# Kernel optimization log

Measured on AMD Instinct MI355X. Metric: run time of the kernel, lower is better.

## Reference

```python
import jax, jax.numpy as jnp
import numpy as np

B, L, D_MODEL, D_STATE, D_HIDDEN = 4, 4096, 1024, 256, 4096
RMIN, RMAX, MAX_PHASE = 0.8, 0.95, 2.0 * np.pi


def setup_inputs() -> dict:
    key = jax.random.key(0)
    ks = jax.random.split(key, 10)
    # LRU ring init (Orvieto et al.): |lambda| in [rmin, rmax], phase in [0, max_phase)
    u1 = jax.random.uniform(ks[0], (D_STATE,))
    u2 = jax.random.uniform(ks[1], (D_STATE,))
    nu_log = jnp.log(-0.5 * jnp.log(u1 * (RMAX**2 - RMIN**2) + RMIN**2))
    theta_log = jnp.log(MAX_PHASE * u2)
    B_re = jax.random.normal(ks[2], (D_STATE, D_MODEL)) / np.sqrt(2.0 * D_MODEL)
    B_im = jax.random.normal(ks[3], (D_STATE, D_MODEL)) / np.sqrt(2.0 * D_MODEL)
    C_re = jax.random.normal(ks[4], (D_MODEL, D_STATE)) / np.sqrt(D_STATE)
    C_im = jax.random.normal(ks[5], (D_MODEL, D_STATE)) / np.sqrt(D_STATE)
    D_mat = jax.random.normal(ks[6], (D_MODEL, D_MODEL)) / np.sqrt(D_MODEL)
    W1 = jax.random.normal(ks[7], (D_MODEL, D_HIDDEN)) * np.sqrt(2.0 / D_MODEL)
    W2 = jax.random.normal(ks[8], (D_HIDDEN, D_MODEL)) * np.sqrt(2.0 / D_HIDDEN)
    res_logit = jnp.asarray(-1.0, dtype=jnp.float32)
    x3d = jax.random.normal(ks[9], (B, L, D_MODEL), dtype=jnp.float32)
    return {"x3d": x3d, "nu_log": nu_log, "theta_log": theta_log,
            "B_re": B_re, "B_im": B_im, "C_re": C_re, "C_im": C_im,
            "D_mat": D_mat, "W1": W1, "W2": W2, "res_logit": res_logit}


def _lru_scan(lam, Bu):
    # diagonal linear recurrence x_t = lam * x_{t-1} + Bu_t via associative scan
    lam_b = jnp.broadcast_to(lam, Bu.shape)  # [B, L, N]

    def comb(a, b):
        return (a[0] * b[0], b[0] * a[1] + b[1])

    _, states = jax.lax.associative_scan(comb, (lam_b, Bu), axis=1)
    return states  # [B, L, N] complex


def reference(x3d, nu_log, theta_log, B_re, B_im, C_re, C_im, D_mat, W1, W2, res_logit):
    lam = jnp.exp(-jnp.exp(nu_log) + 1j * jnp.exp(theta_log))          # [N]
    gamma = jnp.sqrt(1.0 - jnp.abs(lam) ** 2)                           # [N]
    Bn = (gamma[:, None] * (B_re + 1j * B_im))                          # [N, D]
    Bu = jnp.einsum('bld,nd->bln', x3d.astype(jnp.complex64), Bn)       # [B, L, N]
    states = _lru_scan(lam.astype(jnp.complex64), Bu)                   # [B, L, N]
    y = jnp.einsum('bln,mn->blm', states, C_re + 1j * C_im).real \
        + jnp.einsum('bld,md->blm', x3d, D_mat)                         # [B, L, D]
    # MLP feedforward (nl_layers=2, bias=False), dropout is identity at p=0
    z = jax.nn.gelu(y @ W1) @ W2                                        # [B, L, D]
    out = x3d + jax.nn.sigmoid(res_logit) * z
    st = states[:, -1]  # final recurrent state
    return out, st
```

## Files before the change

kernel.cpp:

```cpp
#include <hip/hip_runtime.h>
#include <stdint.h>

typedef __bf16 bf16;
typedef bf16 bf16x8 __attribute__((ext_vector_type(8)));
typedef float f32x4 __attribute__((ext_vector_type(4)));

#define B_  4
#define L_  4096
#define DM  1024
#define DS  256
#define DH  4096
#define BL  16384
#define CL  64
#define NC  64

__device__ __forceinline__ float bfbits(uint32_t lo16) {
  union { uint32_t u; float f; } v; v.u = lo16 << 16; return v.f;
}

__device__ __forceinline__ void async16(const bf16* g, bf16* l) {
  __builtin_amdgcn_global_load_lds(
      (const __attribute__((address_space(1))) uint32_t*)g,
      (__attribute__((address_space(3))) uint32_t*)l, 16, 0, 0);
}

#define MEMFENCE()  asm volatile("" ::: "memory")
#define LGKM0()     asm volatile("s_waitcnt lgkmcnt(0)" ::: "memory")
#define SCHEDB()    __builtin_amdgcn_sched_barrier(0)

__global__ void phaseA(const float* __restrict__ nu_log,
                       const float* __restrict__ th_log,
                       float* __restrict__ scal) {
  int n = threadIdx.x;
  float nu = __expf(nu_log[n]);
  float th = __expf(th_log[n]);
  float mod = __expf(-nu);
  float lr = mod * cosf(th);
  float li = mod * sinf(th);
  float g = sqrtf(fmaxf(1.0f - mod * mod, 0.0f));
  float pr = 1.f, pi = 0.f;
  for (int i = 0; i < CL; i++) {
    float nr = pr * lr - pi * li;
    float ni = pr * li + pi * lr;
    pr = nr; pi = ni;
  }
  scal[n] = lr; scal[256 + n] = li;
  scal[512 + n] = pr; scal[768 + n] = pi;
  scal[1024 + n] = g;
}

__global__ void prep_bu(const float* __restrict__ B_re, const float* __restrict__ B_im,
                        const float* __restrict__ scal, bf16* __restrict__ WB) {
  size_t i = (size_t)blockIdx.x * 256 + threadIdx.x;
  int row = (int)(i >> 10), col = (int)(i & 1023);
  int n = row >> 1;
  const float* src = (row & 1) ? B_im : B_re;
  WB[i] = (bf16)(scal[1024 + n] * src[n * 1024 + col]);
}

__global__ void prep_y(const float* __restrict__ C_re, const float* __restrict__ C_im,
                       const float* __restrict__ D_mat, bf16* __restrict__ WB) {
  size_t i = (size_t)blockIdx.x * 256 + threadIdx.x;
  int m = (int)(i / 1536), c = (int)(i % 1536);
  float v;
  if (c < 256)       v = C_re[m * 256 + c];
  else if (c < 512)  v = -C_im[m * 256 + (c - 256)];
  else               v = D_mat[m * 1024 + (c - 512)];
  WB[i] = (bf16)v;
}

__global__ void transpose_to_bf16(const float* __restrict__ in, bf16* __restrict__ out,
                                  int R, int C) {
  __shared__ float tile[32][33];
  int c0 = blockIdx.x * 32, r0 = blockIdx.y * 32;
  int tx = threadIdx.x, ty = threadIdx.y;
  for (int i = 0; i < 32; i += 8)
    tile[ty + i][tx] = in[(size_t)(r0 + ty + i) * C + c0 + tx];
  __syncthreads();
  for (int i = 0; i < 32; i += 8)
    out[(size_t)(c0 + ty + i) * R + r0 + tx] = (bf16)tile[tx][ty + i];
}

__global__ void conv_x(const float4* __restrict__ x, bf16* __restrict__ XS) {
  size_t i = (size_t)blockIdx.x * 256 + threadIdx.x;
  size_t t = i >> 8;
  int d4 = (int)(i & 255);
  float4 v = x[i];
  bf16* o = XS + t * 1536 + 512 + (size_t)d4 * 4;
  o[0] = (bf16)v.x; o[1] = (bf16)v.y; o[2] = (bf16)v.z; o[3] = (bf16)v.w;
}

template <int EPI>
__device__ __forceinline__ void epi_store(void* C, int ldc, size_t row, size_t col,
                                          float v, float sig, const float* xres) {
  size_t off = row * (size_t)ldc + col;
  if (EPI == 0) {
    ((bf16*)C)[off] = (bf16)v;
  } else if (EPI == 1) {
    float z = 0.7978845608f * (v + 0.044715f * v * v * v);
    float gv = v / (1.f + __expf(-2.f * z));
    ((bf16*)C)[off] = (bf16)gv;
  } else {
    ((float*)C)[off] = xres[off] + sig * v;
  }
}

template <int EPI>
__global__ __launch_bounds__(512, 2) void gemm256(
    const bf16* __restrict__ A, int lda,
    const bf16* __restrict__ Bt, int ldb,
    void* __restrict__ C, int ldc, int NK, int mt, int nt,
    const float* __restrict__ xres, const float* __restrict__ reslog) {
  __shared__ __align__(16) bf16 sA[2 * 16384];
  __shared__ __align__(16) bf16 sB[2 * 16384];

  const int tid  = threadIdx.x;
  const int lane = tid & 63;
  const int wave = tid >> 6;
  const int q = lane >> 4, l16 = lane & 15;
  const int wr = wave >> 2, wc = wave & 3;

  int nb = mt * nt;
  int per = nb >> 3;
  int t0 = (blockIdx.x & 7) * per + (blockIdx.x >> 3);
  int gsz = nt << 3;
  int g = t0 / gsz, r = t0 % gsz;
  size_t m0 = (size_t)(g * 8 + (r & 7)) * 256;
  size_t n0 = (size_t)(r >> 3) * 256;

  const int srow = tid >> 3;
  const int scol = (((tid & 7) ^ ((tid >> 3) & 7)) << 3);
  const bf16* gA = A  + (m0 + srow) * (size_t)lda + scol;
  const bf16* gB = Bt + (n0 + srow) * (size_t)ldb + scol;
  bf16* lA = sA + tid * 8;
  bf16* lB = sB + tid * 8;

  auto stageA = [&](int kt) {
    const bf16* s = gA + kt * 64;
    bf16* l = lA + (kt & 1) * 16384;
    async16(s, l);
    async16(s + (size_t)64  * lda, l + 4096);
    async16(s + (size_t)128 * lda, l + 8192);
    async16(s + (size_t)192 * lda, l + 12288);
  };
  auto stageB = [&](int kt) {
    const bf16* s = gB + kt * 64;
    bf16* l = lB + (kt & 1) * 16384;
    async16(s, l);
    async16(s + (size_t)64  * ldb, l + 4096);
    async16(s + (size_t)128 * ldb, l + 8192);
    async16(s + (size_t)192 * ldb, l + 12288);
  };

  stageA(0); stageB(0); stageA(1); stageB(1);
  __builtin_amdgcn_s_waitcnt(0x0F78);
  __builtin_amdgcn_s_barrier();
  MEMFENCE();

  const int sw  = (l16 & 7) << 3;
  const int qx0 = (q << 3) ^ sw;
  const int qx1 = ((q << 3) + 32) ^ sw;
  const bf16* Ard = sA + wr * 8192 + l16 * 64;
  const bf16* Brd = sB + (wc >> 1) * 8192 + ((wc & 1) * 64 + l16) * 64;

  f32x4 acc[8][4] = {};
  bf16x8 a0[4], a1[4], b0[4], b1[4];

#pragma unroll
  for (int j = 0; j < 4; ++j) a0[j] = *(const bf16x8*)&Ard[j * 1024 + qx0];
#pragma unroll
  for (int n = 0; n < 4; ++n) b0[n] = *(const bf16x8*)&Brd[n * 1024 + qx0];

  for (int kt = 0; kt < NK; ++kt) {
    const bf16* Ab  = Ard + (kt & 1) * 16384;
    const bf16* Bb  = Brd + (kt & 1) * 16384;
    const bf16* Abn = Ard + ((kt + 1) & 1) * 16384;
    const bf16* Bbn = Brd + ((kt + 1) & 1) * 16384;

#pragma unroll
    for (int j = 0; j < 4; ++j) a1[j] = *(const bf16x8*)&Ab[j * 1024 + qx1];
#pragma unroll
    for (int n = 0; n < 4; ++n) b1[n] = *(const bf16x8*)&Bb[n * 1024 + qx1];
    SCHEDB();
    __builtin_amdgcn_s_setprio(1);
#pragma unroll
    for (int j = 0; j < 4; ++j)
#pragma unroll
      for (int n = 0; n < 4; ++n)
        acc[j][n] = __builtin_amdgcn_mfma_f32_16x16x32_bf16(a0[j], b0[n], acc[j][n], 0, 0, 0);
    __builtin_amdgcn_s_setprio(0);

#pragma unroll
    for (int j = 0; j < 4; ++j) a0[j] = *(const bf16x8*)&Ab[(4 + j) * 1024 + qx0];
    SCHEDB();
    __builtin_amdgcn_s_setprio(1);
#pragma unroll
    for (int j = 0; j < 4; ++j)
#pragma unroll
      for (int n = 0; n < 4; ++n)
        acc[j][n] = __builtin_amdgcn_mfma_f32_16x16x32_bf16(a1[j], b1[n], acc[j][n], 0, 0, 0);
    __builtin_amdgcn_s_setprio(0);

#pragma unroll
    for (int j = 0; j < 4; ++j) a1[j] = *(const bf16x8*)&Ab[(4 + j) * 1024 + qx1];
    SCHEDB();
    __builtin_amdgcn_s_setprio(1);
#pragma unroll
    for (int j = 0; j < 4; ++j)
#pragma unroll
      for (int n = 0; n < 4; ++n)
        acc[4 + j][n] = __builtin_amdgcn_mfma_f32_16x16x32_bf16(a0[j], b0[n], acc[4 + j][n], 0, 0, 0);
    __builtin_amdgcn_s_setprio(0);

    MEMFENCE();
    __builtin_amdgcn_s_waitcnt(0x0F70);
    LGKM0();
    __builtin_amdgcn_s_barrier();
    MEMFENCE();

    if (kt + 1 < NK) {
#pragma unroll
      for (int j = 0; j < 4; ++j) a0[j] = *(const bf16x8*)&Abn[j * 1024 + qx0];
#pragma unroll
      for (int n = 0; n < 4; ++n) b0[n] = *(const bf16x8*)&Bbn[n * 1024 + qx0];
    }
    if (kt + 2 < NK) { stageA(kt + 2); stageB(kt + 2); }
    SCHEDB();
    __builtin_amdgcn_s_setprio(1);
#pragma unroll
    for (int j = 0; j < 4; ++j)
#pragma unroll
      for (int n = 0; n < 4; ++n)
        acc[4 + j][n] = __builtin_amdgcn_mfma_f32_16x16x32_bf16(a1[j], b1[n], acc[4 + j][n], 0, 0, 0);
    __builtin_amdgcn_s_setprio(0);
  }

  float sig = 0.f;
  if (EPI == 2) sig = 1.f / (1.f + __expf(-reslog[0]));
#pragma unroll
  for (int mi = 0; mi < 8; ++mi)
#pragma unroll
    for (int ni = 0; ni < 4; ++ni) {
      size_t col = n0 + wc * 64 + ni * 16 + l16;
#pragma unroll
      for (int r2 = 0; r2 < 4; ++r2) {
        size_t row = m0 + wr * 128 + mi * 16 + q * 4 + r2;
        epi_store<EPI>(C, ldc, row, col, acc[mi][ni][r2], sig, xres);
      }
    }
}

template <int EPI>
__global__ __launch_bounds__(512, 2) void gemm128(
    const bf16* __restrict__ A, int lda,
    const bf16* __restrict__ Bt, int ldb,
    void* __restrict__ C, int ldc, int NK, int mt, int nt,
    const float* __restrict__ xres, const float* __restrict__ reslog) {
  __shared__ __align__(16) bf16 sA[2 * 8192];
  __shared__ __align__(16) bf16 sB[2 * 16384];

  const int tid  = threadIdx.x;
  const int lane = tid & 63;
  const int wave = tid >> 6;
  const int q = lane >> 4, l16 = lane & 15;
  const int wr = wave >> 2, wc = wave & 3;

  int nb = mt * nt;
  int per = nb >> 3;
  int t0 = (blockIdx.x & 7) * per + (blockIdx.x >> 3);
  int gsz = nt << 3;
  int g = t0 / gsz, r = t0 % gsz;
  size_t m0 = (size_t)(g * 8 + (r & 7)) * 128;
  size_t n0 = (size_t)(r >> 3) * 256;

  const int srow = tid >> 3;
  const int scol = (((tid & 7) ^ ((tid >> 3) & 7)) << 3);
  const bf16* gA = A  + (m0 + srow) * (size_t)lda + scol;
  const bf16* gB = Bt + (n0 + srow) * (size_t)ldb + scol;
  bf16* lA = sA + tid * 8;
  bf16* lB = sB + tid * 8;

  auto stageA = [&](int kt) {
    const bf16* s = gA + kt * 64;
    bf16* l = lA + (kt & 1) * 8192;
    async16(s, l);
    async16(s + (size_t)64 * lda, l + 4096);
  };
  auto stageB = [&](int kt) {
    const bf16* s = gB + kt * 64;
    bf16* l = lB + (kt & 1) * 16384;
    async16(s, l);
    async16(s + (size_t)64  * ldb, l + 4096);
    async16(s + (size_t)128 * ldb, l + 8192);
    async16(s + (size_t)192 * ldb, l + 12288);
  };

  stageA(0); stageB(0); stageA(1); stageB(1);
  __builtin_amdgcn_s_waitcnt(0x0F76);
  __builtin_amdgcn_s_barrier();
  MEMFENCE();

  const int sw  = (l16 & 7) << 3;
  const int qx0 = (q << 3) ^ sw;
  const int qx1 = ((q << 3) + 32) ^ sw;
  const bf16* Ard = sA + (wr * 64 + l16) * 64;
  const bf16* Brd = sB + (wc >> 1) * 8192 + ((wc & 1) * 64 + l16) * 64;

  f32x4 acc[4][4] = {};
  bf16x8 a0[4], a1[4], b0[4], b1[4];

#pragma unroll
  for (int j = 0; j < 4; ++j) a0[j] = *(const bf16x8*)&Ard[j * 1024 + qx0];
#pragma unroll
  for (int n = 0; n < 4; ++n) b0[n] = *(const bf16x8*)&Brd[n * 1024 + qx0];

  for (int kt = 0; kt < NK; ++kt) {
    const bf16* Ab  = Ard + (kt & 1) * 8192;
    const bf16* Bb  = Brd + (kt & 1) * 16384;
    const bf16* Abn = Ard + ((kt + 1) & 1) * 8192;
    const bf16* Bbn = Brd + ((kt + 1) & 1) * 16384;

#pragma unroll
    for (int j = 0; j < 4; ++j) a1[j] = *(const bf16x8*)&Ab[j * 1024 + qx1];
#pragma unroll
    for (int n = 0; n < 4; ++n) b1[n] = *(const bf16x8*)&Bb[n * 1024 + qx1];
    SCHEDB();
    __builtin_amdgcn_s_setprio(1);
#pragma unroll
    for (int j = 0; j < 4; ++j)
#pragma unroll
      for (int n = 0; n < 4; ++n)
        acc[j][n] = __builtin_amdgcn_mfma_f32_16x16x32_bf16(a0[j], b0[n], acc[j][n], 0, 0, 0);
    __builtin_amdgcn_s_setprio(0);

    MEMFENCE();
    __builtin_amdgcn_s_waitcnt(0x0F70);
    LGKM0();
    __builtin_amdgcn_s_barrier();
    MEMFENCE();

    if (kt + 1 < NK) {
#pragma unroll
      for (int j = 0; j < 4; ++j) a0[j] = *(const bf16x8*)&Abn[j * 1024 + qx0];
#pragma unroll
      for (int n = 0; n < 4; ++n) b0[n] = *(const bf16x8*)&Bbn[n * 1024 + qx0];
    }
    if (kt + 2 < NK) { stageA(kt + 2); stageB(kt + 2); }
    SCHEDB();
    __builtin_amdgcn_s_setprio(1);
#pragma unroll
    for (int j = 0; j < 4; ++j)
#pragma unroll
      for (int n = 0; n < 4; ++n)
        acc[j][n] = __builtin_amdgcn_mfma_f32_16x16x32_bf16(a1[j], b1[n], acc[j][n], 0, 0, 0);
    __builtin_amdgcn_s_setprio(0);
  }

  float sig = 0.f;
  if (EPI == 2) sig = 1.f / (1.f + __expf(-reslog[0]));
#pragma unroll
  for (int mi = 0; mi < 4; ++mi)
#pragma unroll
    for (int ni = 0; ni < 4; ++ni) {
      size_t col = n0 + wc * 64 + ni * 16 + l16;
#pragma unroll
      for (int r2 = 0; r2 < 4; ++r2) {
        size_t row = m0 + wr * 64 + mi * 16 + q * 4 + r2;
        epi_store<EPI>(C, ldc, row, col, acc[mi][ni][r2], sig, xres);
      }
    }
}

__global__ void scan_pass1(const bf16* __restrict__ Bu, const float* __restrict__ scal,
                           float2* __restrict__ H) {
  int b = blockIdx.x >> 6, c = blockIdx.x & 63, n = threadIdx.x;
  float lr = scal[n], li = scal[256 + n];
  float sr = 0.f, si = 0.f;
  size_t t0 = (size_t)b * L_ + (size_t)c * CL;
  const uint32_t* p = (const uint32_t*)(Bu + t0 * 512) + n;
  for (int j = 0; j < CL; j++) {
    uint32_t u = p[(size_t)j * 256];
    float ur = bfbits(u & 0xffffu), ui = bfbits(u >> 16);
    float nr = lr * sr - li * si + ur;
    float ni = lr * si + li * sr + ui;
    sr = nr; si = ni;
  }
  H[(size_t)(b * NC + c) * 256 + n] = make_float2(sr, si);
}

__global__ void scan_pass2(const float2* __restrict__ H, const float* __restrict__ scal,
                           float2* __restrict__ Carry) {
  int b = blockIdx.x, n = threadIdx.x;
  float Pr = scal[512 + n], Pi = scal[768 + n];
  float cr = 0.f, ci = 0.f;
  for (int c = 0; c < NC; c++) {
    Carry[(size_t)(b * NC + c) * 256 + n] = make_float2(cr, ci);
    float2 h = H[(size_t)(b * NC + c) * 256 + n];
    float nr = Pr * cr - Pi * ci + h.x;
    float ni = Pr * ci + Pi * cr + h.y;
    cr = nr; ci = ni;
  }
}

__global__ void scan_pass3(const bf16* __restrict__ Bu, const float* __restrict__ scal,
                           const float2* __restrict__ Carry, bf16* __restrict__ XS,
                           float* __restrict__ st) {
  int b = blockIdx.x >> 6, c = blockIdx.x & 63, n = threadIdx.x;
  float lr = scal[n], li = scal[256 + n];
  float2 cv = Carry[(size_t)(b * NC + c) * 256 + n];
  float sr = cv.x, si = cv.y;
  size_t t0 = (size_t)b * L_ + (size_t)c * CL;
  const uint32_t* p = (const uint32_t*)(Bu + t0 * 512) + n;
  bf16* qp = XS + t0 * 1536 + n;
  for (int j = 0; j < CL; j++) {
    uint32_t u = p[(size_t)j * 256];
    float ur = bfbits(u & 0xffffu), ui = bfbits(u >> 16);
    float nr = lr * sr - li * si + ur;
    float ni = lr * si + li * sr + ui;
    sr = nr; si = ni;
    qp[(size_t)j * 1536] = (bf16)sr;
    qp[(size_t)j * 1536 + 256] = (bf16)si;
  }
  if (c == NC - 1) {
    st[(size_t)b * 256 + n] = sr;
    st[1024 + (size_t)b * 256 + n] = si;
  }
}

extern "C" void kernel_launch(void* const* d_in, const int* in_sizes, int n_in,
                              void* d_out, int out_size, void* d_ws, size_t ws_size,
                              hipStream_t stream) {
  const float* x      = (const float*)d_in[0];
  const float* nu_log = (const float*)d_in[1];
  const float* th_log = (const float*)d_in[2];
  const float* B_re   = (const float*)d_in[3];
  const float* B_im   = (const float*)d_in[4];
  const float* C_re   = (const float*)d_in[5];
  const float* C_im   = (const float*)d_in[6];
  const float* D_mat  = (const float*)d_in[7];
  const float* W1     = (const float*)d_in[8];
  const float* W2     = (const float*)d_in[9];
  const float* reslog = (const float*)d_in[10];

  char* wsb = (char*)d_ws;
  size_t off = 0;
  auto alloc = [&](size_t bytes) {
    void* p = wsb + off;
    off += (bytes + 255) & ~(size_t)255;
    return p;
  };
  float*  scal = (float*)alloc(5 * 256 * 4);
  bf16*   WBbu = (bf16*)alloc((size_t)512 * 1024 * 2);
  bf16*   WBy  = (bf16*)alloc((size_t)1024 * 1536 * 2);
  bf16*   WB1  = (bf16*)alloc((size_t)4096 * 1024 * 2);
  bf16*   WB2  = (bf16*)alloc((size_t)1024 * 4096 * 2);
  float2* H    = (float2*)alloc((size_t)B_ * NC * 256 * 8);
  float2* Cr   = (float2*)alloc((size_t)B_ * NC * 256 * 8);
  bf16*   Ybf  = (bf16*)alloc((size_t)BL * 1024 * 2);
  bf16*   XS   = (bf16*)alloc((size_t)BL * 1536 * 2);
  bf16*   Bu   = (bf16*)alloc((size_t)BL * 512 * 2);
  bf16*   Hbf  = XS;

  float* out = (float*)d_out;
  float* st  = out + (size_t)BL * DM;

  phaseA<<<1, 256, 0, stream>>>(nu_log, th_log, scal);
  prep_bu<<<512 * 1024 / 256, 256, 0, stream>>>(B_re, B_im, scal, WBbu);
  prep_y<<<1024 * 1536 / 256, 256, 0, stream>>>(C_re, C_im, D_mat, WBy);
  transpose_to_bf16<<<dim3(4096 / 32, 1024 / 32), dim3(32, 8), 0, stream>>>(W1, WB1, 1024, 4096);
  transpose_to_bf16<<<dim3(1024 / 32, 4096 / 32), dim3(32, 8), 0, stream>>>(W2, WB2, 4096, 1024);
  conv_x<<<BL * 256 / 256, 256, 0, stream>>>((const float4*)x, XS);

  gemm128<0><<<128 * 2, 512, 0, stream>>>(
      XS + 512, 1536, WBbu, 1024, Bu, 512, 16, 128, 2, nullptr, nullptr);

  scan_pass1<<<B_ * NC, 256, 0, stream>>>(Bu, scal, H);
  scan_pass2<<<B_, 256, 0, stream>>>(H, scal, Cr);
  scan_pass3<<<B_ * NC, 256, 0, stream>>>(Bu, scal, Cr, XS, st);

  gemm256<0><<<64 * 4, 512, 0, stream>>>(
      XS, 1536, WBy, 1536, Ybf, 1024, 24, 64, 4, nullptr, nullptr);

  for (int i = 0; i < 2; i++) {
    const bf16* Yc = Ybf + (size_t)i * 8192 * 1024;
    float* Oc = out + (size_t)i * 8192 * 1024;
    const float* Xc = x + (size_t)i * 8192 * 1024;
    gemm256<1><<<32 * 16, 512, 0, stream>>>(
        Yc, 1024, WB1, 1024, Hbf, 4096, 16, 32, 16, nullptr, nullptr);
    gemm128<2><<<64 * 4, 512, 0, stream>>>(
        Hbf, 4096, WB2, 4096, Oc, 1024, 64, 64, 4, Xc, reslog);
  }
}
```

Measured before the change: 555.9 us.

## Fuse prep kernels into one launch and rework gemm256 to 4-wave 128x128 warp tiles

The six preprocessing kernels (lambda scalars, B/C/D weight packing, W1/W2 transposes, x conversion) become one launch that dispatches on block index. The BU-weight blocks recompute gamma locally, so they no longer depend on the scalar block. gemm256 moves from 8 waves with 64x... tiles and a hand-scheduled, setprio-interleaved double buffer to 4 waves, each computing 128x128 with 64 accumulators. It stages the next K tile during compute and uses one __syncthreads per iteration. This removes launch overhead and raises per-wave register reuse, at the cost of heavy register pressure, fewer waves to hide latency, and a possible LDS race: the next tile is staged into the other buffer before all waves have finished reading it.

```diff
diff --git a/kernel.cpp b/kernel.cpp
--- a/kernel.cpp
+++ b/kernel.cpp
@@ -26,68 +26,71 @@
 
 #define MEMFENCE()  asm volatile("" ::: "memory")
 #define LGKM0()     asm volatile("s_waitcnt lgkmcnt(0)" ::: "memory")
+#define MFMA16(a, b, c) __builtin_amdgcn_mfma_f32_16x16x32_bf16((a), (b), (c), 0, 0, 0)
 #define SCHEDB()    __builtin_amdgcn_sched_barrier(0)
 
-__global__ void phaseA(const float* __restrict__ nu_log,
-                       const float* __restrict__ th_log,
-                       float* __restrict__ scal) {
-  int n = threadIdx.x;
-  float nu = __expf(nu_log[n]);
-  float th = __expf(th_log[n]);
-  float mod = __expf(-nu);
-  float lr = mod * cosf(th);
-  float li = mod * sinf(th);
-  float g = sqrtf(fmaxf(1.0f - mod * mod, 0.0f));
-  float pr = 1.f, pi = 0.f;
-  for (int i = 0; i < CL; i++) {
-    float nr = pr * lr - pi * li;
-    float ni = pr * li + pi * lr;
-    pr = nr; pi = ni;
-  }
-  scal[n] = lr; scal[256 + n] = li;
-  scal[512 + n] = pr; scal[768 + n] = pi;
-  scal[1024 + n] = g;
-}
-
-__global__ void prep_bu(const float* __restrict__ B_re, const float* __restrict__ B_im,
-                        const float* __restrict__ scal, bf16* __restrict__ WB) {
-  size_t i = (size_t)blockIdx.x * 256 + threadIdx.x;
-  int row = (int)(i >> 10), col = (int)(i & 1023);
-  int n = row >> 1;
-  const float* src = (row & 1) ? B_im : B_re;
-  WB[i] = (bf16)(scal[1024 + n] * src[n * 1024 + col]);
-}
-
-__global__ void prep_y(const float* __restrict__ C_re, const float* __restrict__ C_im,
-                       const float* __restrict__ D_mat, bf16* __restrict__ WB) {
-  size_t i = (size_t)blockIdx.x * 256 + threadIdx.x;
-  int m = (int)(i / 1536), c = (int)(i % 1536);
-  float v;
-  if (c < 256)       v = C_re[m * 256 + c];
-  else if (c < 512)  v = -C_im[m * 256 + (c - 256)];
-  else               v = D_mat[m * 1024 + (c - 512)];
-  WB[i] = (bf16)v;
-}
-
-__global__ void transpose_to_bf16(const float* __restrict__ in, bf16* __restrict__ out,
-                                  int R, int C) {
+__global__ void prep_fused(const float4* __restrict__ x, bf16* __restrict__ XS,
+                           const float* __restrict__ C_re, const float* __restrict__ C_im,
+                           const float* __restrict__ D_mat, bf16* __restrict__ WBy,
+                           const float* __restrict__ B_re, const float* __restrict__ B_im,
+                           const float* __restrict__ nu_log, const float* __restrict__ th_log,
+                           bf16* __restrict__ WBbu,
+                           const float* __restrict__ W1, bf16* __restrict__ WB1,
+                           const float* __restrict__ W2, bf16* __restrict__ WB2,
+                           float* __restrict__ scal) {
   __shared__ float tile[32][33];
-  int c0 = blockIdx.x * 32, r0 = blockIdx.y * 32;
-  int tx = threadIdx.x, ty = threadIdx.y;
-  for (int i = 0; i < 32; i += 8)
-    tile[ty + i][tx] = in[(size_t)(r0 + ty + i) * C + c0 + tx];
-  __syncthreads();
-  for (int i = 0; i < 32; i += 8)
-    out[(size_t)(c0 + ty + i) * R + r0 + tx] = (bf16)tile[tx][ty + i];
-}
-
-__global__ void conv_x(const float4* __restrict__ x, bf16* __restrict__ XS) {
-  size_t i = (size_t)blockIdx.x * 256 + threadIdx.x;
-  size_t t = i >> 8;
-  int d4 = (int)(i & 255);
-  float4 v = x[i];
-  bf16* o = XS + t * 1536 + 512 + (size_t)d4 * 4;
-  o[0] = (bf16)v.x; o[1] = (bf16)v.y; o[2] = (bf16)v.z; o[3] = (bf16)v.w;
+  int bid = blockIdx.x, tid = threadIdx.x;
+  if (bid < 16384) {
+    size_t i = (size_t)bid * 256 + tid;
+    size_t t = i >> 8;
+    int d4 = (int)(i & 255);
+    float4 v = x[i];
+    bf16* o = XS + t * 1536 + 512 + (size_t)d4 * 4;
+    o[0] = (bf16)v.x; o[1] = (bf16)v.y; o[2] = (bf16)v.z; o[3] = (bf16)v.w;
+  } else if (bid < 22528) {
+    size_t i = (size_t)(bid - 16384) * 256 + tid;
+    int m = (int)(i / 1536), c = (int)(i % 1536);
+    float v;
+    if (c < 256)       v = C_re[m * 256 + c];
+    else if (c < 512)  v = -C_im[m * 256 + (c - 256)];
+    else               v = D_mat[m * 1024 + (c - 512)];
+    WBy[i] = (bf16)v;
+  } else if (bid < 24576) {
+    size_t i = (size_t)(bid - 22528) * 256 + tid;
+    int row = (int)(i >> 10), col = (int)(i & 1023);
+    int n = row >> 1;
+    float mod = __expf(-__expf(nu_log[n]));
+    float g = sqrtf(fmaxf(1.0f - mod * mod, 0.0f));
+    const float* src = (row & 1) ? B_im : B_re;
+    WBbu[i] = (bf16)(g * src[n * 1024 + col]);
+  } else if (bid < 32768) {
+    const float* in; bf16* out; int R, C, bx, by;
+    if (bid < 28672) { int t = bid - 24576; in = W1; out = WB1; R = 1024; C = 4096; bx = t & 127; by = t >> 7; }
+    else             { int t = bid - 28672; in = W2; out = WB2; R = 4096; C = 1024; bx = t & 31;  by = t >> 5; }
+    int c0 = bx * 32, r0 = by * 32, tx = tid & 31, ty = tid >> 5;
+    for (int i = 0; i < 32; i += 8)
+      tile[ty + i][tx] = in[(size_t)(r0 + ty + i) * C + c0 + tx];
+    __syncthreads();
+    for (int i = 0; i < 32; i += 8)
+      out[(size_t)(c0 + ty + i) * R + r0 + tx] = (bf16)tile[tx][ty + i];
+  } else {
+    int n = tid;
+    float nu = __expf(nu_log[n]);
+    float th = __expf(th_log[n]);
+    float mod = __expf(-nu);
+    float lr = mod * cosf(th);
+    float li = mod * sinf(th);
+    float g = sqrtf(fmaxf(1.0f - mod * mod, 0.0f));
+    float pr = 1.f, pi = 0.f;
+    for (int i = 0; i < CL; i++) {
+      float nr = pr * lr - pi * li;
+      float ni = pr * li + pi * lr;
+      pr = nr; pi = ni;
+    }
+    scal[n] = lr; scal[256 + n] = li;
+    scal[512 + n] = pr; scal[768 + n] = pi;
+    scal[1024 + n] = g;
+  }
 }
 
 template <int EPI>
@@ -106,7 +109,7 @@
 }
 
 template <int EPI>
-__global__ __launch_bounds__(512, 2) void gemm256(
+__global__ __launch_bounds__(256, 1) void gemm256(
     const bf16* __restrict__ A, int lda,
     const bf16* __restrict__ Bt, int ldb,
     void* __restrict__ C, int ldc, int NK, int mt, int nt,
@@ -118,7 +121,7 @@
   const int lane = tid & 63;
   const int wave = tid >> 6;
   const int q = lane >> 4, l16 = lane & 15;
-  const int wr = wave >> 2, wc = wave & 3;
+  const int wr = wave >> 1, wc = wave & 1;
 
   int nb = mt * nt;
   int per = nb >> 3;
@@ -138,101 +141,57 @@
   auto stageA = [&](int kt) {
     const bf16* s = gA + kt * 64;
     bf16* l = lA + (kt & 1) * 16384;
-    async16(s, l);
-    async16(s + (size_t)64  * lda, l + 4096);
-    async16(s + (size_t)128 * lda, l + 8192);
-    async16(s + (size_t)192 * lda, l + 12288);
+#pragma unroll
+    for (int u = 0; u < 8; ++u)
+      async16(s + (size_t)(u * 32) * lda, l + u * 2048);
   };
   auto stageB = [&](int kt) {
     const bf16* s = gB + kt * 64;
     bf16* l = lB + (kt & 1) * 16384;
-    async16(s, l);
-    async16(s + (size_t)64  * ldb, l + 4096);
-    async16(s + (size_t)128 * ldb, l + 8192);
-    async16(s + (size_t)192 * ldb, l + 12288);
+#pragma unroll
+    for (int u = 0; u < 8; ++u)
+      async16(s + (size_t)(u * 32) * ldb, l + u * 2048);
   };
 
-  stageA(0); stageB(0); stageA(1); stageB(1);
-  __builtin_amdgcn_s_waitcnt(0x0F78);
-  __builtin_amdgcn_s_barrier();
-  MEMFENCE();
+  stageA(0); stageB(0);
+  __syncthreads();
 
   const int sw  = (l16 & 7) << 3;
   const int qx0 = (q << 3) ^ sw;
   const int qx1 = ((q << 3) + 32) ^ sw;
-  const bf16* Ard = sA + wr * 8192 + l16 * 64;
-  const bf16* Brd = sB + (wc >> 1) * 8192 + ((wc & 1) * 64 + l16) * 64;
-
-  f32x4 acc[8][4] = {};
-  bf16x8 a0[4], a1[4], b0[4], b1[4];
-
-#pragma unroll
-  for (int j = 0; j < 4; ++j) a0[j] = *(const bf16x8*)&Ard[j * 1024 + qx0];
-#pragma unroll
-  for (int n = 0; n < 4; ++n) b0[n] = *(const bf16x8*)&Brd[n * 1024 + qx0];
+  const bf16* Ard = sA + (wr * 128 + l16) * 64;
+  const bf16* Brd = sB + (wc * 128 + l16) * 64;
+
+  f32x4 acc[8][8] = {};
+  bf16x8 a[8], b[8];
 
   for (int kt = 0; kt < NK; ++kt) {
-    const bf16* Ab  = Ard + (kt & 1) * 16384;
-    const bf16* Bb  = Brd + (kt & 1) * 16384;
-    const bf16* Abn = Ard + ((kt + 1) & 1) * 16384;
-    const bf16* Bbn = Brd + ((kt + 1) & 1) * 16384;
-
-#pragma unroll
-    for (int j = 0; j < 4; ++j) a1[j] = *(const bf16x8*)&Ab[j * 1024 + qx1];
-#pragma unroll
-    for (int n = 0; n < 4; ++n) b1[n] = *(const bf16x8*)&Bb[n * 1024 + qx1];
-    SCHEDB();
-    __builtin_amdgcn_s_setprio(1);
-#pragma unroll
-    for (int j = 0; j < 4; ++j)
-#pragma unroll
-      for (int n = 0; n < 4; ++n)
-        acc[j][n] = __builtin_amdgcn_mfma_f32_16x16x32_bf16(a0[j], b0[n], acc[j][n], 0, 0, 0);
-    __builtin_amdgcn_s_setprio(0);
-
-#pragma unroll
-    for (int j = 0; j < 4; ++j) a0[j] = *(const bf16x8*)&Ab[(4 + j) * 1024 + qx0];
-    SCHEDB();
-    __builtin_amdgcn_s_setprio(1);
-#pragma unroll
-    for (int j = 0; j < 4; ++j)
-#pragma unroll
-      for (int n = 0; n < 4; ++n)
-        acc[j][n] = __builtin_amdgcn_mfma_f32_16x16x32_bf16(a1[j], b1[n], acc[j][n], 0, 0, 0);
-    __builtin_amdgcn_s_setprio(0);
-
-#pragma unroll
-    for (int j = 0; j < 4; ++j) a1[j] = *(const bf16x8*)&Ab[(4 + j) * 1024 + qx1];
-    SCHEDB();
-    __builtin_amdgcn_s_setprio(1);
-#pragma unroll
-    for (int j = 0; j < 4; ++j)
-#pragma unroll
-      for (int n = 0; n < 4; ++n)
-        acc[4 + j][n] = __builtin_amdgcn_mfma_f32_16x16x32_bf16(a0[j], b0[n], acc[4 + j][n], 0, 0, 0);
-    __builtin_amdgcn_s_setprio(0);
-
-    MEMFENCE();
-    __builtin_amdgcn_s_waitcnt(0x0F70);
-    LGKM0();
-    __builtin_amdgcn_s_barrier();
-    MEMFENCE();
-
-    if (kt + 1 < NK) {
-#pragma unroll
-      for (int j = 0; j < 4; ++j) a0[j] = *(const bf16x8*)&Abn[j * 1024 + qx0];
-#pragma unroll
-      for (int n = 0; n < 4; ++n) b0[n] = *(const bf16x8*)&Bbn[n * 1024 + qx0];
-    }
-    if (kt + 2 < NK) { stageA(kt + 2); stageB(kt + 2); }
-    SCHEDB();
-    __builtin_amdgcn_s_setprio(1);
-#pragma unroll
-    for (int j = 0; j < 4; ++j)
-#pragma unroll
-      for (int n = 0; n < 4; ++n)
-        acc[4 + j][n] = __builtin_amdgcn_mfma_f32_16x16x32_bf16(a1[j], b1[n], acc[4 + j][n], 0, 0, 0);
-    __builtin_amdgcn_s_setprio(0);
+    const bf16* Ab = Ard + (kt & 1) * 16384;
+    const bf16* Bb = Brd + (kt & 1) * 16384;
+
+#pragma unroll
+    for (int m = 0; m < 8; ++m) a[m] = *(const bf16x8*)&Ab[m * 1024 + qx0];
+#pragma unroll
+    for (int n = 0; n < 8; ++n) b[n] = *(const bf16x8*)&Bb[n * 1024 + qx0];
+    if (kt + 1 < NK) stageA(kt + 1);
+#pragma unroll
+    for (int m = 0; m < 8; ++m)
+#pragma unroll
+      for (int n = 0; n < 8; ++n)
+        acc[m][n] = MFMA16(a[m], b[n], acc[m][n]);
+
+#pragma unroll
+    for (int m = 0; m < 8; ++m) a[m] = *(const bf16x8*)&Ab[m * 1024 + qx1];
+#pragma unroll
+    for (int n = 0; n < 8; ++n) b[n] = *(const bf16x8*)&Bb[n * 1024 + qx1];
+    if (kt + 1 < NK) stageB(kt + 1);
+#pragma unroll
+    for (int m = 0; m < 8; ++m)
+#pragma unroll
+      for (int n = 0; n < 8; ++n)
+        acc[m][n] = MFMA16(a[m], b[n], acc[m][n]);
+
+    __syncthreads();
   }
 
   float sig = 0.f;
@@ -240,8 +199,8 @@
 #pragma unroll
   for (int mi = 0; mi < 8; ++mi)
 #pragma unroll
-    for (int ni = 0; ni < 4; ++ni) {
-      size_t col = n0 + wc * 64 + ni * 16 + l16;
+    for (int ni = 0; ni < 8; ++ni) {
+      size_t col = n0 + wc * 128 + ni * 16 + l16;
 #pragma unroll
       for (int r2 = 0; r2 < 4; ++r2) {
         size_t row = m0 + wr * 128 + mi * 16 + q * 4 + r2;
@@ -330,7 +289,7 @@
     for (int j = 0; j < 4; ++j)
 #pragma unroll
       for (int n = 0; n < 4; ++n)
-        acc[j][n] = __builtin_amdgcn_mfma_f32_16x16x32_bf16(a0[j], b0[n], acc[j][n], 0, 0, 0);
+        acc[j][n] = MFMA16(a0[j], b0[n], acc[j][n]);
     __builtin_amdgcn_s_setprio(0);
 
     MEMFENCE();
@@ -352,7 +311,7 @@
     for (int j = 0; j < 4; ++j)
 #pragma unroll
       for (int n = 0; n < 4; ++n)
-        acc[j][n] = __builtin_amdgcn_mfma_f32_16x16x32_bf16(a1[j], b1[n], acc[j][n], 0, 0, 0);
+        acc[j][n] = MFMA16(a1[j], b1[n], acc[j][n]);
     __builtin_amdgcn_s_setprio(0);
   }
 
@@ -464,12 +423,9 @@
   float* out = (float*)d_out;
   float* st  = out + (size_t)BL * DM;
 
-  phaseA<<<1, 256, 0, stream>>>(nu_log, th_log, scal);
-  prep_bu<<<512 * 1024 / 256, 256, 0, stream>>>(B_re, B_im, scal, WBbu);
-  prep_y<<<1024 * 1536 / 256, 256, 0, stream>>>(C_re, C_im, D_mat, WBy);
-  transpose_to_bf16<<<dim3(4096 / 32, 1024 / 32), dim3(32, 8), 0, stream>>>(W1, WB1, 1024, 4096);
-  transpose_to_bf16<<<dim3(1024 / 32, 4096 / 32), dim3(32, 8), 0, stream>>>(W2, WB2, 4096, 1024);
-  conv_x<<<BL * 256 / 256, 256, 0, stream>>>((const float4*)x, XS);
+  prep_fused<<<32769, 256, 0, stream>>>(
+      (const float4*)x, XS, C_re, C_im, D_mat, WBy,
+      B_re, B_im, nu_log, th_log, WBbu, W1, WB1, W2, WB2, scal);
 
   gemm128<0><<<128 * 2, 512, 0, stream>>>(
       XS + 512, 1536, WBbu, 1024, Bu, 512, 16, 128, 2, nullptr, nullptr);
@@ -478,14 +434,14 @@
   scan_pass2<<<B_, 256, 0, stream>>>(H, scal, Cr);
   scan_pass3<<<B_ * NC, 256, 0, stream>>>(Bu, scal, Cr, XS, st);
 
-  gemm256<0><<<64 * 4, 512, 0, stream>>>(
+  gemm256<0><<<64 * 4, 256, 0, stream>>>(
       XS, 1536, WBy, 1536, Ybf, 1024, 24, 64, 4, nullptr, nullptr);
 
   for (int i = 0; i < 2; i++) {
     const bf16* Yc = Ybf + (size_t)i * 8192 * 1024;
     float* Oc = out + (size_t)i * 8192 * 1024;
     const float* Xc = x + (size_t)i * 8192 * 1024;
-    gemm256<1><<<32 * 16, 512, 0, stream>>>(
+    gemm256<1><<<32 * 16, 256, 0, stream>>>(
         Yc, 1024, WB1, 1024, Hbf, 4096, 16, 32, 16, nullptr, nullptr);
     gemm128<2><<<64 * 4, 512, 0, stream>>>(
         Hbf, 4096, WB2, 4096, Oc, 1024, 64, 64, 4, Xc, reslog);
```

Result: slower. 642.0 us (+15.5%).
